# Performance work log

Hardware: AMD Instinct MI355X
Metric: run time of the kernel (lower is better)

Reference implementation:

```python
import jax, jax.numpy as jnp
import numpy as np
from jax.scipy.special import logsumexp

B, N, D, H = 8, 2048, 3, 256
BLUR = 0.001            # geomloss blur
EPS0 = 32.0             # ~diameter^2/2 for unit-std gaussian clouds
N_ITERS = 14            # eps-scaling steps down to blur^2
EPS_LIST = np.geomspace(EPS0, BLUR ** 2, N_ITERS).astype(np.float32)


def _sqdist(x, y):
    # x: [B,N,3], y: [B,M,3] -> [B,N,M] squared euclidean distance
    x2 = jnp.sum(x * x, -1)[:, :, None]
    y2 = jnp.sum(y * y, -1)[:, None, :]
    xy = jnp.einsum('bnd,bmd->bnm', x, y)
    return jnp.maximum(x2 + y2 - 2.0 * xy, 0.0)


def sinkhorn_potential_g(x, y):
    """Log-domain Sinkhorn (p=2 cost ||x-y||^2/2, uniform weights) with
    epsilon scaling; returns second dual potential g over y. Mimics
    geomloss.SamplesLoss('sinkhorn', p=2, blur=0.001, potentials=True)."""
    C = 0.5 * _sqdist(x, y)                      # [B,N,M]
    n, m = x.shape[1], y.shape[1]
    loga = -jnp.log(jnp.float32(n))
    logb = -jnp.log(jnp.float32(m))
    f = jnp.zeros((x.shape[0], n), C.dtype)
    g = jnp.zeros((x.shape[0], m), C.dtype)
    for eps in EPS_LIST:
        f = -eps * logsumexp(logb + (g[:, None, :] - C) / eps, axis=2)
        g = -eps * logsumexp(loga + (f[:, :, None] - C) / eps, axis=1)
    return g


def get_hard_assignment(x, y):
    # idx such that y[idx] is the OT match for x
    g = sinkhorn_potential_g(x, y)                       # [B,M]
    C_minus_g = _sqdist(x, y) - g[:, None, :]            # [B,N,M]
    return jnp.argmin(C_minus_g, axis=2)                 # [B,N]


def setup_inputs() -> dict:
    key = jax.random.key(0)
    ks = jax.random.split(key, 8)
    return {
        'cloud': jax.random.normal(ks[0], (B, N, D), jnp.float32),
        'noise': jax.random.normal(ks[1], (B, N, D), jnp.float32),
        't': jax.random.uniform(ks[2], (B,), jnp.float32),
        'W1': jax.random.normal(ks[3], (D, H), jnp.float32) * 0.1,
        'Wt': jax.random.normal(ks[4], (H,), jnp.float32) * 0.1,
        'b1': jnp.zeros((H,), jnp.float32),
        'W2': jax.random.normal(ks[5], (H, D), jnp.float32) * 0.1,
        'b2': jnp.zeros((D,), jnp.float32),
    }


def reference(cloud, noise, t, W1, Wt, b1, W2, b2):
    # std normalization (torch.std -> unbiased, ddof=1), done under no_grad
    std = jnp.std(cloud, axis=(1, 2), keepdims=True, ddof=1)
    x0 = cloud / std
    idx = get_hard_assignment(noise, x0)                 # [B,N] int
    x0_aligned = jnp.take_along_axis(x0, idx[:, :, None], axis=1)  # [B,N,3]
    tv = t[:, None, None]
    x_t = (1.0 - tv) * x0_aligned + tv * noise
    # stand-in diffusion network: per-point MLP conditioned on t
    h = jax.nn.relu(jnp.einsum('bnd,dh->bnh', x_t, W1) + tv * Wt + b1)
    v_pred = jnp.einsum('bnh,hd->bnd', h, W2) + b2
    v = noise - x0_aligned
    return v_pred, v
```

## Files before the change

kernel.cpp:

```cpp
#include <hip/hip_runtime.h>
#include <math.h>

#define B_ 8
#define N_ 2048
#define D_ 3
#define H_ 256
#define ND_ (N_*D_)
#define BN_ (B_*N_)

__global__ __launch_bounds__(256) void std_kernel(const float* __restrict__ cloud,
                                                  float* __restrict__ stdv) {
  __shared__ float red[256];
  int b = blockIdx.x, tid = threadIdx.x;
  const float* p = cloud + (size_t)b * ND_;
  float s = 0.f;
  for (int i = tid; i < ND_; i += 256) s += p[i];
  red[tid] = s; __syncthreads();
  for (int off = 128; off > 0; off >>= 1) {
    if (tid < off) red[tid] += red[tid + off];
    __syncthreads();
  }
  float mean = red[0] / (float)ND_;
  __syncthreads();
  float ss = 0.f;
  for (int i = tid; i < ND_; i += 256) { float d = p[i] - mean; ss += d * d; }
  red[tid] = ss; __syncthreads();
  for (int off = 128; off > 0; off >>= 1) {
    if (tid < off) red[tid] += red[tid + off];
    __syncthreads();
  }
  if (tid == 0) stdv[b] = sqrtf(red[0] / (float)(ND_ - 1));
}

__global__ __launch_bounds__(256) void prep_kernel(const float* __restrict__ cloud,
    const float* __restrict__ noise, const float* __restrict__ stdv,
    float4* __restrict__ x0p, float4* __restrict__ np4,
    float* __restrict__ f, float* __restrict__ g) {
  int i = blockIdx.x * 256 + threadIdx.x;
  if (i >= BN_) return;
  int b = i >> 11;
  float sd = stdv[b];
  float cx = cloud[3*i] / sd, cy = cloud[3*i+1] / sd, cz = cloud[3*i+2] / sd;
  x0p[i] = make_float4(cx, cy, cz, cx*cx + cy*cy + cz*cz);
  float ax = noise[3*i], ay = noise[3*i+1], az = noise[3*i+2];
  np4[i] = make_float4(ax, ay, az, ax*ax + ay*ay + az*az);
  f[i] = 0.f; g[i] = 0.f;
}

__global__ __launch_bounds__(256, 2) void lse_kernel(
    const float4* __restrict__ outer, const float4* __restrict__ inner,
    const float* __restrict__ pin, float* __restrict__ pout,
    float scl, float kk, float hh, float c1, float c2) {
  __shared__ float4 sP[N_];
  int tid = threadIdx.x;
  int b = blockIdx.x >> 7;
  int rowBase = (blockIdx.x & 127) << 4;
  int base = b * N_;
  for (int j = tid; j < N_; j += 256) {
    float4 p = inner[base + j];
    float q = kk * pin[base + j] - hh * p.w;
    sP[j] = make_float4(scl * p.x, scl * p.y, scl * p.z, q);
  }
  __syncthreads();
  int wave = tid >> 6, lane = tid & 63;
  int r0 = base + rowBase + (wave << 2);
  float4 A0 = outer[r0], A1 = outer[r0+1], A2 = outer[r0+2], A3 = outer[r0+3];
  float a0x = scl*A0.x, a0y = scl*A0.y, a0z = scl*A0.z, rc0 = -hh*A0.w;
  float a1x = scl*A1.x, a1y = scl*A1.y, a1z = scl*A1.z, rc1 = -hh*A1.w;
  float a2x = scl*A2.x, a2y = scl*A2.y, a2z = scl*A2.z, rc2 = -hh*A2.w;
  float a3x = scl*A3.x, a3y = scl*A3.y, a3z = scl*A3.z, rc3 = -hh*A3.w;
  float v0[32], v1[32], v2[32], v3[32];
  float m0 = -INFINITY, m1 = -INFINITY, m2 = -INFINITY, m3 = -INFINITY;
#pragma unroll
  for (int jj = 0; jj < 32; ++jj) {
    float4 p = sP[(jj << 6) + lane];
    float t0 = fmaf(p.x, a0x, p.w); t0 = fmaf(p.y, a0y, t0); t0 = fmaf(p.z, a0z, t0);
    v0[jj] = t0; m0 = fmaxf(m0, t0);
    float t1 = fmaf(p.x, a1x, p.w); t1 = fmaf(p.y, a1y, t1); t1 = fmaf(p.z, a1z, t1);
    v1[jj] = t1; m1 = fmaxf(m1, t1);
    float t2 = fmaf(p.x, a2x, p.w); t2 = fmaf(p.y, a2y, t2); t2 = fmaf(p.z, a2z, t2);
    v2[jj] = t2; m2 = fmaxf(m2, t2);
    float t3 = fmaf(p.x, a3x, p.w); t3 = fmaf(p.y, a3y, t3); t3 = fmaf(p.z, a3z, t3);
    v3[jj] = t3; m3 = fmaxf(m3, t3);
  }
#pragma unroll
  for (int off = 32; off >= 1; off >>= 1) {
    m0 = fmaxf(m0, __shfl_xor(m0, off, 64));
    m1 = fmaxf(m1, __shfl_xor(m1, off, 64));
    m2 = fmaxf(m2, __shfl_xor(m2, off, 64));
    m3 = fmaxf(m3, __shfl_xor(m3, off, 64));
  }
  float s0 = 0.f, s1 = 0.f, s2 = 0.f, s3 = 0.f;
#pragma unroll
  for (int jj = 0; jj < 32; ++jj) {
    s0 += __builtin_amdgcn_exp2f(v0[jj] - m0);
    s1 += __builtin_amdgcn_exp2f(v1[jj] - m1);
    s2 += __builtin_amdgcn_exp2f(v2[jj] - m2);
    s3 += __builtin_amdgcn_exp2f(v3[jj] - m3);
  }
#pragma unroll
  for (int off = 32; off >= 1; off >>= 1) {
    s0 += __shfl_xor(s0, off, 64);
    s1 += __shfl_xor(s1, off, 64);
    s2 += __shfl_xor(s2, off, 64);
    s3 += __shfl_xor(s3, off, 64);
  }
  if (lane == 0) {
    pout[r0]   = fmaf(c1, rc0 + m0 + __builtin_amdgcn_logf(s0), c2);
    pout[r0+1] = fmaf(c1, rc1 + m1 + __builtin_amdgcn_logf(s1), c2);
    pout[r0+2] = fmaf(c1, rc2 + m2 + __builtin_amdgcn_logf(s2), c2);
    pout[r0+3] = fmaf(c1, rc3 + m3 + __builtin_amdgcn_logf(s3), c2);
  }
}

__global__ __launch_bounds__(256) void assign_mlp_kernel(
    const float4* __restrict__ np4, const float4* __restrict__ x0p,
    const float* __restrict__ g, const float* __restrict__ t,
    const float* __restrict__ W1, const float* __restrict__ Wt,
    const float* __restrict__ b1, const float* __restrict__ W2,
    const float* __restrict__ b2, float* __restrict__ out) {
  __shared__ float4 sPts[N_];
  __shared__ float  sg[N_];
  __shared__ float  sW1[3*H_], sWt[H_], sb1[H_], sW2[H_*3], sb2[3];
  int tid = threadIdx.x;
  int b = blockIdx.x >> 8;
  int rowBase = (blockIdx.x & 255) << 3;
  int base = b * N_;
  for (int j = tid; j < N_; j += 256) { sPts[j] = x0p[base+j]; sg[j] = g[base+j]; }
  for (int i = tid; i < 3*H_; i += 256) { sW1[i] = W1[i]; sW2[i] = W2[i]; }
  if (tid < H_) { sWt[tid] = Wt[tid]; sb1[tid] = b1[tid]; }
  if (tid < 3) sb2[tid] = b2[tid];
  __syncthreads();
  int wave = tid >> 6, lane = tid & 63;
  float tb = t[b];
  for (int rr = 0; rr < 2; ++rr) {
    int r = rowBase + (wave << 1) + rr;
    float4 A = np4[base + r];
    float best = INFINITY; int bidx = 0;
#pragma unroll
    for (int jj = 0; jj < 32; ++jj) {
      int j = (jj << 6) + lane;
      float4 p = sPts[j];
      float d = A.x*p.x + A.y*p.y + A.z*p.z;
      float val = fmaxf(A.w + p.w - 2.0f*d, 0.0f) - sg[j];
      if (val < best) { best = val; bidx = j; }
    }
#pragma unroll
    for (int off = 32; off >= 1; off >>= 1) {
      float ov = __shfl_xor(best, off, 64);
      int   oi = __shfl_xor(bidx, off, 64);
      if (ov < best || (ov == best && oi < bidx)) { best = ov; bidx = oi; }
    }
    float4 xa = sPts[bidx];
    float xtx = (1.0f - tb)*xa.x + tb*A.x;
    float xty = (1.0f - tb)*xa.y + tb*A.y;
    float xtz = (1.0f - tb)*xa.z + tb*A.z;
    float acc0 = 0.f, acc1 = 0.f, acc2 = 0.f;
#pragma unroll
    for (int hh = 0; hh < 4; ++hh) {
      int h = (hh << 6) + lane;
      float hv = xtx*sW1[h] + xty*sW1[H_+h] + xtz*sW1[2*H_+h] + tb*sWt[h] + sb1[h];
      hv = fmaxf(hv, 0.0f);
      acc0 += hv * sW2[3*h];
      acc1 += hv * sW2[3*h+1];
      acc2 += hv * sW2[3*h+2];
    }
#pragma unroll
    for (int off = 32; off >= 1; off >>= 1) {
      acc0 += __shfl_xor(acc0, off, 64);
      acc1 += __shfl_xor(acc1, off, 64);
      acc2 += __shfl_xor(acc2, off, 64);
    }
    if (lane == 0) {
      int gi = base + r;
      out[3*gi]   = acc0 + sb2[0];
      out[3*gi+1] = acc1 + sb2[1];
      out[3*gi+2] = acc2 + sb2[2];
      out[3*BN_ + 3*gi]   = A.x - xa.x;
      out[3*BN_ + 3*gi+1] = A.y - xa.y;
      out[3*BN_ + 3*gi+2] = A.z - xa.z;
    }
  }
}

extern "C" void kernel_launch(void* const* d_in, const int* in_sizes, int n_in,
                              void* d_out, int out_size, void* d_ws, size_t ws_size,
                              hipStream_t stream) {
  (void)in_sizes; (void)n_in; (void)out_size; (void)ws_size;
  const float* cloud = (const float*)d_in[0];
  const float* noise = (const float*)d_in[1];
  const float* t     = (const float*)d_in[2];
  const float* W1    = (const float*)d_in[3];
  const float* Wt    = (const float*)d_in[4];
  const float* b1    = (const float*)d_in[5];
  const float* W2    = (const float*)d_in[6];
  const float* b2w   = (const float*)d_in[7];
  float* out = (float*)d_out;

  float* ws   = (float*)d_ws;
  float* stdv = ws;
  float4* x0p = (float4*)(ws + 16);
  float4* np4 = (float4*)(ws + 16 + 4*BN_);
  float* f    = ws + 16 + 8*BN_;
  float* g    = f + BN_;

  std_kernel<<<B_, 256, 0, stream>>>(cloud, stdv);
  prep_kernel<<<BN_/256, 256, 0, stream>>>(cloud, noise, stdv, x0p, np4, f, g);

  const double LOG2E = 1.4426950408889634074;
  const double LN2   = 0.6931471805599453094;
  const double logw  = -log(2048.0);
  const double l0 = log10(32.0), l1 = log10(1e-6);
  for (int kit = 0; kit < 14; ++kit) {
    double epsd = pow(10.0, l0 + (l1 - l0) * ((double)kit / 13.0));
    float eps = (float)epsd;
    float kk  = (float)(LOG2E / (double)eps);
    float hh  = 0.5f * kk;
    float scl = sqrtf(kk);
    float c1  = (float)(-(double)eps * LN2);
    float c2  = (float)(-(double)eps * logw);
    lse_kernel<<<B_*(N_/16), 256, 0, stream>>>(np4, x0p, g, f, scl, kk, hh, c1, c2);
    lse_kernel<<<B_*(N_/16), 256, 0, stream>>>(x0p, np4, f, g, scl, kk, hh, c1, c2);
  }

  assign_mlp_kernel<<<B_*(N_/8), 256, 0, stream>>>(np4, x0p, g, t, W1, Wt, b1, W2, b2w, out);
}
```

Measured before the change: 415.8 us.

## Recompute LSE logits instead of storing, raise occupancy, split argmin and MLP

The LSE kernel no longer keeps 128 logits per thread in registers. It recomputes the three FMAs per element in the exp pass, which lets launch bounds target 4 blocks per CU instead of 2. The row-point loads are hoisted above the shared-memory fill. The final kernel is split into an argmin kernel (16 rows per block, writes x_t to workspace) and a per-point MLP kernel with one thread per point, which removes the wave-wide shuffle reductions. The cost is extra FMAs and shared reads in the LSE loop and one more launch plus a workspace round trip.

```diff
diff --git a/kernel.cpp b/kernel.cpp
--- a/kernel.cpp
+++ b/kernel.cpp
@@ -47,7 +47,7 @@
   f[i] = 0.f; g[i] = 0.f;
 }
 
-__global__ __launch_bounds__(256, 2) void lse_kernel(
+__global__ __launch_bounds__(256, 4) void lse_kernel(
     const float4* __restrict__ outer, const float4* __restrict__ inner,
     const float* __restrict__ pin, float* __restrict__ pout,
     float scl, float kk, float hh, float c1, float c2) {
@@ -56,32 +56,31 @@
   int b = blockIdx.x >> 7;
   int rowBase = (blockIdx.x & 127) << 4;
   int base = b * N_;
+  int wave = tid >> 6, lane = tid & 63;
+  int r0 = base + rowBase + (wave << 2);
+  float4 A0 = outer[r0], A1 = outer[r0+1], A2 = outer[r0+2], A3 = outer[r0+3];
   for (int j = tid; j < N_; j += 256) {
     float4 p = inner[base + j];
     float q = kk * pin[base + j] - hh * p.w;
     sP[j] = make_float4(scl * p.x, scl * p.y, scl * p.z, q);
   }
-  __syncthreads();
-  int wave = tid >> 6, lane = tid & 63;
-  int r0 = base + rowBase + (wave << 2);
-  float4 A0 = outer[r0], A1 = outer[r0+1], A2 = outer[r0+2], A3 = outer[r0+3];
   float a0x = scl*A0.x, a0y = scl*A0.y, a0z = scl*A0.z, rc0 = -hh*A0.w;
   float a1x = scl*A1.x, a1y = scl*A1.y, a1z = scl*A1.z, rc1 = -hh*A1.w;
   float a2x = scl*A2.x, a2y = scl*A2.y, a2z = scl*A2.z, rc2 = -hh*A2.w;
   float a3x = scl*A3.x, a3y = scl*A3.y, a3z = scl*A3.z, rc3 = -hh*A3.w;
-  float v0[32], v1[32], v2[32], v3[32];
+  __syncthreads();
   float m0 = -INFINITY, m1 = -INFINITY, m2 = -INFINITY, m3 = -INFINITY;
 #pragma unroll
   for (int jj = 0; jj < 32; ++jj) {
     float4 p = sP[(jj << 6) + lane];
     float t0 = fmaf(p.x, a0x, p.w); t0 = fmaf(p.y, a0y, t0); t0 = fmaf(p.z, a0z, t0);
-    v0[jj] = t0; m0 = fmaxf(m0, t0);
+    m0 = fmaxf(m0, t0);
     float t1 = fmaf(p.x, a1x, p.w); t1 = fmaf(p.y, a1y, t1); t1 = fmaf(p.z, a1z, t1);
-    v1[jj] = t1; m1 = fmaxf(m1, t1);
+    m1 = fmaxf(m1, t1);
     float t2 = fmaf(p.x, a2x, p.w); t2 = fmaf(p.y, a2y, t2); t2 = fmaf(p.z, a2z, t2);
-    v2[jj] = t2; m2 = fmaxf(m2, t2);
+    m2 = fmaxf(m2, t2);
     float t3 = fmaf(p.x, a3x, p.w); t3 = fmaf(p.y, a3y, t3); t3 = fmaf(p.z, a3z, t3);
-    v3[jj] = t3; m3 = fmaxf(m3, t3);
+    m3 = fmaxf(m3, t3);
   }
 #pragma unroll
   for (int off = 32; off >= 1; off >>= 1) {
@@ -93,10 +92,15 @@
   float s0 = 0.f, s1 = 0.f, s2 = 0.f, s3 = 0.f;
 #pragma unroll
   for (int jj = 0; jj < 32; ++jj) {
-    s0 += __builtin_amdgcn_exp2f(v0[jj] - m0);
-    s1 += __builtin_amdgcn_exp2f(v1[jj] - m1);
-    s2 += __builtin_amdgcn_exp2f(v2[jj] - m2);
-    s3 += __builtin_amdgcn_exp2f(v3[jj] - m3);
+    float4 p = sP[(jj << 6) + lane];
+    float t0 = fmaf(p.x, a0x, p.w); t0 = fmaf(p.y, a0y, t0); t0 = fmaf(p.z, a0z, t0);
+    s0 += __builtin_amdgcn_exp2f(t0 - m0);
+    float t1 = fmaf(p.x, a1x, p.w); t1 = fmaf(p.y, a1y, t1); t1 = fmaf(p.z, a1z, t1);
+    s1 += __builtin_amdgcn_exp2f(t1 - m1);
+    float t2 = fmaf(p.x, a2x, p.w); t2 = fmaf(p.y, a2y, t2); t2 = fmaf(p.z, a2z, t2);
+    s2 += __builtin_amdgcn_exp2f(t2 - m2);
+    float t3 = fmaf(p.x, a3x, p.w); t3 = fmaf(p.y, a3y, t3); t3 = fmaf(p.z, a3z, t3);
+    s3 += __builtin_amdgcn_exp2f(t3 - m3);
   }
 #pragma unroll
   for (int off = 32; off >= 1; off >>= 1) {
@@ -113,36 +117,34 @@
   }
 }
 
-__global__ __launch_bounds__(256) void assign_mlp_kernel(
+__global__ __launch_bounds__(256, 4) void argmin_kernel(
     const float4* __restrict__ np4, const float4* __restrict__ x0p,
     const float* __restrict__ g, const float* __restrict__ t,
-    const float* __restrict__ W1, const float* __restrict__ Wt,
-    const float* __restrict__ b1, const float* __restrict__ W2,
-    const float* __restrict__ b2, float* __restrict__ out) {
+    float4* __restrict__ xt4, float* __restrict__ out) {
   __shared__ float4 sPts[N_];
   __shared__ float  sg[N_];
-  __shared__ float  sW1[3*H_], sWt[H_], sb1[H_], sW2[H_*3], sb2[3];
   int tid = threadIdx.x;
-  int b = blockIdx.x >> 8;
-  int rowBase = (blockIdx.x & 255) << 3;
+  int b = blockIdx.x >> 7;
+  int rowBase = (blockIdx.x & 127) << 4;
   int base = b * N_;
+  int wave = tid >> 6, lane = tid & 63;
+  int r0 = base + rowBase + (wave << 2);
+  float4 A[4];
+#pragma unroll
+  for (int i = 0; i < 4; ++i) A[i] = np4[r0 + i];
   for (int j = tid; j < N_; j += 256) { sPts[j] = x0p[base+j]; sg[j] = g[base+j]; }
-  for (int i = tid; i < 3*H_; i += 256) { sW1[i] = W1[i]; sW2[i] = W2[i]; }
-  if (tid < H_) { sWt[tid] = Wt[tid]; sb1[tid] = b1[tid]; }
-  if (tid < 3) sb2[tid] = b2[tid];
-  __syncthreads();
-  int wave = tid >> 6, lane = tid & 63;
+  __syncthreads();
   float tb = t[b];
-  for (int rr = 0; rr < 2; ++rr) {
-    int r = rowBase + (wave << 1) + rr;
-    float4 A = np4[base + r];
+#pragma unroll
+  for (int rr = 0; rr < 4; ++rr) {
+    float4 Ar = A[rr];
     float best = INFINITY; int bidx = 0;
 #pragma unroll
     for (int jj = 0; jj < 32; ++jj) {
       int j = (jj << 6) + lane;
       float4 p = sPts[j];
-      float d = A.x*p.x + A.y*p.y + A.z*p.z;
-      float val = fmaxf(A.w + p.w - 2.0f*d, 0.0f) - sg[j];
+      float d = Ar.x*p.x + Ar.y*p.y + Ar.z*p.z;
+      float val = fmaxf(Ar.w + p.w - 2.0f*d, 0.0f) - sg[j];
       if (val < best) { best = val; bidx = j; }
     }
 #pragma unroll
@@ -151,36 +153,46 @@
       int   oi = __shfl_xor(bidx, off, 64);
       if (ov < best || (ov == best && oi < bidx)) { best = ov; bidx = oi; }
     }
-    float4 xa = sPts[bidx];
-    float xtx = (1.0f - tb)*xa.x + tb*A.x;
-    float xty = (1.0f - tb)*xa.y + tb*A.y;
-    float xtz = (1.0f - tb)*xa.z + tb*A.z;
-    float acc0 = 0.f, acc1 = 0.f, acc2 = 0.f;
-#pragma unroll
-    for (int hh = 0; hh < 4; ++hh) {
-      int h = (hh << 6) + lane;
-      float hv = xtx*sW1[h] + xty*sW1[H_+h] + xtz*sW1[2*H_+h] + tb*sWt[h] + sb1[h];
-      hv = fmaxf(hv, 0.0f);
-      acc0 += hv * sW2[3*h];
-      acc1 += hv * sW2[3*h+1];
-      acc2 += hv * sW2[3*h+2];
+    if (lane == 0) {
+      float4 xa = sPts[bidx];
+      int gi = r0 + rr;
+      float xtx = (1.0f - tb)*xa.x + tb*Ar.x;
+      float xty = (1.0f - tb)*xa.y + tb*Ar.y;
+      float xtz = (1.0f - tb)*xa.z + tb*Ar.z;
+      xt4[gi] = make_float4(xtx, xty, xtz, 0.0f);
+      out[3*BN_ + 3*gi]   = Ar.x - xa.x;
+      out[3*BN_ + 3*gi+1] = Ar.y - xa.y;
+      out[3*BN_ + 3*gi+2] = Ar.z - xa.z;
     }
-#pragma unroll
-    for (int off = 32; off >= 1; off >>= 1) {
-      acc0 += __shfl_xor(acc0, off, 64);
-      acc1 += __shfl_xor(acc1, off, 64);
-      acc2 += __shfl_xor(acc2, off, 64);
-    }
-    if (lane == 0) {
-      int gi = base + r;
-      out[3*gi]   = acc0 + sb2[0];
-      out[3*gi+1] = acc1 + sb2[1];
-      out[3*gi+2] = acc2 + sb2[2];
-      out[3*BN_ + 3*gi]   = A.x - xa.x;
-      out[3*BN_ + 3*gi+1] = A.y - xa.y;
-      out[3*BN_ + 3*gi+2] = A.z - xa.z;
-    }
-  }
+  }
+}
+
+__global__ __launch_bounds__(256) void mlp_kernel(
+    const float4* __restrict__ xt4, const float* __restrict__ t,
+    const float* __restrict__ W1, const float* __restrict__ Wt,
+    const float* __restrict__ b1, const float* __restrict__ W2,
+    const float* __restrict__ b2, float* __restrict__ out) {
+  __shared__ float sW1[3*H_], sWt[H_], sb1[H_], sW2[H_*3], sb2[4];
+  int tid = threadIdx.x;
+  for (int i = tid; i < 3*H_; i += 256) { sW1[i] = W1[i]; sW2[i] = W2[i]; }
+  sWt[tid] = Wt[tid]; sb1[tid] = b1[tid];
+  if (tid < 3) sb2[tid] = b2[tid];
+  __syncthreads();
+  int gi = blockIdx.x * 256 + tid;
+  float4 x = xt4[gi];
+  float tb = t[gi >> 11];
+  float acc0 = 0.f, acc1 = 0.f, acc2 = 0.f;
+#pragma unroll 8
+  for (int h = 0; h < H_; ++h) {
+    float hv = x.x*sW1[h] + x.y*sW1[H_+h] + x.z*sW1[2*H_+h] + tb*sWt[h] + sb1[h];
+    hv = fmaxf(hv, 0.0f);
+    acc0 += hv * sW2[3*h];
+    acc1 += hv * sW2[3*h+1];
+    acc2 += hv * sW2[3*h+2];
+  }
+  out[3*gi]   = acc0 + sb2[0];
+  out[3*gi+1] = acc1 + sb2[1];
+  out[3*gi+2] = acc2 + sb2[2];
 }
 
 extern "C" void kernel_launch(void* const* d_in, const int* in_sizes, int n_in,
@@ -203,6 +215,7 @@
   float4* np4 = (float4*)(ws + 16 + 4*BN_);
   float* f    = ws + 16 + 8*BN_;
   float* g    = f + BN_;
+  float4* xt4 = (float4*)(g + BN_);
 
   std_kernel<<<B_, 256, 0, stream>>>(cloud, stdv);
   prep_kernel<<<BN_/256, 256, 0, stream>>>(cloud, noise, stdv, x0p, np4, f, g);
@@ -223,5 +236,6 @@
     lse_kernel<<<B_*(N_/16), 256, 0, stream>>>(x0p, np4, f, g, scl, kk, hh, c1, c2);
   }
 
-  assign_mlp_kernel<<<B_*(N_/8), 256, 0, stream>>>(np4, x0p, g, t, W1, Wt, b1, W2, b2w, out);
-}
+  argmin_kernel<<<B_*(N_/16), 256, 0, stream>>>(np4, x0p, g, t, xt4, out);
+  mlp_kernel<<<BN_/256, 256, 0, stream>>>(xt4, t, W1, Wt, b1, W2, b2w, out);
+}
```

Result: slower. 749.7 us (+80.3%).

## Split argmin and MLP into separate kernels with per-thread MLP rows

Applied to the files above, without the earlier changes.

Splits the combined assignment+MLP kernel into an argmin kernel and a separate MLP kernel. The argmin kernel now handles 4 rows per wave, so each shared-memory point load is reused across rows. It writes the interpolated x_t to a new workspace buffer. The MLP kernel gives each thread one point and loops over the 256 hidden units, reading packed float4 weights from shared memory, which replaces the per-row cross-lane reductions. This adds one kernel launch and a global round trip through the x_t buffer.

```diff
diff --git a/kernel.cpp b/kernel.cpp
--- a/kernel.cpp
+++ b/kernel.cpp
@@ -113,74 +113,105 @@
   }
 }
 
-__global__ __launch_bounds__(256) void assign_mlp_kernel(
+__global__ __launch_bounds__(256, 4) void argmin_kernel(
     const float4* __restrict__ np4, const float4* __restrict__ x0p,
     const float* __restrict__ g, const float* __restrict__ t,
-    const float* __restrict__ W1, const float* __restrict__ Wt,
-    const float* __restrict__ b1, const float* __restrict__ W2,
-    const float* __restrict__ b2, float* __restrict__ out) {
+    float4* __restrict__ xt4, float* __restrict__ out) {
   __shared__ float4 sPts[N_];
   __shared__ float  sg[N_];
-  __shared__ float  sW1[3*H_], sWt[H_], sb1[H_], sW2[H_*3], sb2[3];
   int tid = threadIdx.x;
-  int b = blockIdx.x >> 8;
-  int rowBase = (blockIdx.x & 255) << 3;
+  int b = blockIdx.x >> 7;
+  int rowBase = (blockIdx.x & 127) << 4;
   int base = b * N_;
   for (int j = tid; j < N_; j += 256) { sPts[j] = x0p[base+j]; sg[j] = g[base+j]; }
-  for (int i = tid; i < 3*H_; i += 256) { sW1[i] = W1[i]; sW2[i] = W2[i]; }
-  if (tid < H_) { sWt[tid] = Wt[tid]; sb1[tid] = b1[tid]; }
-  if (tid < 3) sb2[tid] = b2[tid];
   __syncthreads();
   int wave = tid >> 6, lane = tid & 63;
-  float tb = t[b];
-  for (int rr = 0; rr < 2; ++rr) {
-    int r = rowBase + (wave << 1) + rr;
-    float4 A = np4[base + r];
-    float best = INFINITY; int bidx = 0;
-#pragma unroll
-    for (int jj = 0; jj < 32; ++jj) {
-      int j = (jj << 6) + lane;
-      float4 p = sPts[j];
-      float d = A.x*p.x + A.y*p.y + A.z*p.z;
-      float val = fmaxf(A.w + p.w - 2.0f*d, 0.0f) - sg[j];
-      if (val < best) { best = val; bidx = j; }
-    }
-#pragma unroll
-    for (int off = 32; off >= 1; off >>= 1) {
-      float ov = __shfl_xor(best, off, 64);
-      int   oi = __shfl_xor(bidx, off, 64);
-      if (ov < best || (ov == best && oi < bidx)) { best = ov; bidx = oi; }
-    }
-    float4 xa = sPts[bidx];
-    float xtx = (1.0f - tb)*xa.x + tb*A.x;
-    float xty = (1.0f - tb)*xa.y + tb*A.y;
-    float xtz = (1.0f - tb)*xa.z + tb*A.z;
-    float acc0 = 0.f, acc1 = 0.f, acc2 = 0.f;
-#pragma unroll
-    for (int hh = 0; hh < 4; ++hh) {
-      int h = (hh << 6) + lane;
-      float hv = xtx*sW1[h] + xty*sW1[H_+h] + xtz*sW1[2*H_+h] + tb*sWt[h] + sb1[h];
-      hv = fmaxf(hv, 0.0f);
-      acc0 += hv * sW2[3*h];
-      acc1 += hv * sW2[3*h+1];
-      acc2 += hv * sW2[3*h+2];
-    }
-#pragma unroll
-    for (int off = 32; off >= 1; off >>= 1) {
-      acc0 += __shfl_xor(acc0, off, 64);
-      acc1 += __shfl_xor(acc1, off, 64);
-      acc2 += __shfl_xor(acc2, off, 64);
-    }
-    if (lane == 0) {
-      int gi = base + r;
-      out[3*gi]   = acc0 + sb2[0];
-      out[3*gi+1] = acc1 + sb2[1];
-      out[3*gi+2] = acc2 + sb2[2];
+  int r0 = base + rowBase + (wave << 2);
+  float4 A0 = np4[r0], A1 = np4[r0+1], A2 = np4[r0+2], A3 = np4[r0+3];
+  float b0 = INFINITY, b1v = INFINITY, b2v = INFINITY, b3 = INFINITY;
+  int i0 = 0, i1 = 0, i2 = 0, i3 = 0;
+#pragma unroll
+  for (int jj = 0; jj < 32; ++jj) {
+    int j = (jj << 6) + lane;
+    float4 p = sPts[j];
+    float gj = sg[j];
+    float d0 = A0.x*p.x + A0.y*p.y + A0.z*p.z;
+    float v0 = fmaxf(A0.w + p.w - 2.0f*d0, 0.0f) - gj;
+    if (v0 < b0) { b0 = v0; i0 = j; }
+    float d1 = A1.x*p.x + A1.y*p.y + A1.z*p.z;
+    float v1 = fmaxf(A1.w + p.w - 2.0f*d1, 0.0f) - gj;
+    if (v1 < b1v) { b1v = v1; i1 = j; }
+    float d2 = A2.x*p.x + A2.y*p.y + A2.z*p.z;
+    float v2 = fmaxf(A2.w + p.w - 2.0f*d2, 0.0f) - gj;
+    if (v2 < b2v) { b2v = v2; i2 = j; }
+    float d3 = A3.x*p.x + A3.y*p.y + A3.z*p.z;
+    float v3 = fmaxf(A3.w + p.w - 2.0f*d3, 0.0f) - gj;
+    if (v3 < b3) { b3 = v3; i3 = j; }
+  }
+#pragma unroll
+  for (int off = 32; off >= 1; off >>= 1) {
+    float ov; int oi;
+    ov = __shfl_xor(b0, off, 64);  oi = __shfl_xor(i0, off, 64);
+    if (ov < b0 || (ov == b0 && oi < i0)) { b0 = ov; i0 = oi; }
+    ov = __shfl_xor(b1v, off, 64); oi = __shfl_xor(i1, off, 64);
+    if (ov < b1v || (ov == b1v && oi < i1)) { b1v = ov; i1 = oi; }
+    ov = __shfl_xor(b2v, off, 64); oi = __shfl_xor(i2, off, 64);
+    if (ov < b2v || (ov == b2v && oi < i2)) { b2v = ov; i2 = oi; }
+    ov = __shfl_xor(b3, off, 64);  oi = __shfl_xor(i3, off, 64);
+    if (ov < b3 || (ov == b3 && oi < i3)) { b3 = ov; i3 = oi; }
+  }
+  if (lane == 0) {
+    float tb = t[b];
+    int idx[4] = {i0, i1, i2, i3};
+    float4 Ar[4] = {A0, A1, A2, A3};
+#pragma unroll
+    for (int rr = 0; rr < 4; ++rr) {
+      float4 xa = sPts[idx[rr]];
+      float4 A = Ar[rr];
+      int gi = r0 + rr;
+      float xtx = (1.0f - tb)*xa.x + tb*A.x;
+      float xty = (1.0f - tb)*xa.y + tb*A.y;
+      float xtz = (1.0f - tb)*xa.z + tb*A.z;
+      xt4[gi] = make_float4(xtx, xty, xtz, 0.0f);
       out[3*BN_ + 3*gi]   = A.x - xa.x;
       out[3*BN_ + 3*gi+1] = A.y - xa.y;
       out[3*BN_ + 3*gi+2] = A.z - xa.z;
     }
   }
+}
+
+__global__ __launch_bounds__(128) void mlp_kernel(
+    const float4* __restrict__ xt4, const float* __restrict__ t,
+    const float* __restrict__ W1, const float* __restrict__ Wt,
+    const float* __restrict__ b1, const float* __restrict__ W2,
+    const float* __restrict__ b2, float* __restrict__ out) {
+  __shared__ float4 wA[H_];
+  __shared__ float4 wB[H_];
+  __shared__ float  sb2[4];
+  int tid = threadIdx.x;
+  for (int h = tid; h < H_; h += 128) {
+    wA[h] = make_float4(W1[h], W1[H_+h], W1[2*H_+h], Wt[h]);
+    wB[h] = make_float4(b1[h], W2[3*h], W2[3*h+1], W2[3*h+2]);
+  }
+  if (tid < 3) sb2[tid] = b2[tid];
+  __syncthreads();
+  int gi = blockIdx.x * 128 + tid;
+  float4 x = xt4[gi];
+  float tb = t[gi >> 11];
+  float acc0 = 0.f, acc1 = 0.f, acc2 = 0.f;
+#pragma unroll 4
+  for (int h = 0; h < H_; ++h) {
+    float4 a = wA[h];
+    float4 c = wB[h];
+    float hv = x.x*a.x + x.y*a.y + x.z*a.z + tb*a.w + c.x;
+    hv = fmaxf(hv, 0.0f);
+    acc0 += hv * c.y;
+    acc1 += hv * c.z;
+    acc2 += hv * c.w;
+  }
+  out[3*gi]   = acc0 + sb2[0];
+  out[3*gi+1] = acc1 + sb2[1];
+  out[3*gi+2] = acc2 + sb2[2];
 }
 
 extern "C" void kernel_launch(void* const* d_in, const int* in_sizes, int n_in,
@@ -203,6 +234,7 @@
   float4* np4 = (float4*)(ws + 16 + 4*BN_);
   float* f    = ws + 16 + 8*BN_;
   float* g    = f + BN_;
+  float4* xt4 = (float4*)(g + BN_);
 
   std_kernel<<<B_, 256, 0, stream>>>(cloud, stdv);
   prep_kernel<<<BN_/256, 256, 0, stream>>>(cloud, noise, stdv, x0p, np4, f, g);
@@ -223,5 +255,6 @@
     lse_kernel<<<B_*(N_/16), 256, 0, stream>>>(x0p, np4, f, g, scl, kk, hh, c1, c2);
   }
 
-  assign_mlp_kernel<<<B_*(N_/8), 256, 0, stream>>>(np4, x0p, g, t, W1, Wt, b1, W2, b2w, out);
-}
+  argmin_kernel<<<B_*(N_/16), 256, 0, stream>>>(np4, x0p, g, t, xt4, out);
+  mlp_kernel<<<BN_/128, 128, 0, stream>>>(xt4, t, W1, Wt, b1, W2, b2w, out);
+}
```

Result: slower. 507.7 us (+22.1%).
